# Optimization experiments

Measured on AMD Instinct MI355X. Metric: run time of the kernel, lower is better.

## Reference

```python
import jax, jax.numpy as jnp
import numpy as np

N, C, H, W = 32, 512, 32, 32
D = C // 2  # theta/phi embed channels


def setup_inputs() -> dict:
    key = jax.random.key(0)
    ks = jax.random.split(key, 7)
    s = 0.05
    return {
        "x": jax.random.normal(ks[0], (N, C, H, W), jnp.float32),
        "W_theta": jax.random.normal(ks[1], (D, C), jnp.float32) * s,
        "b_theta": jax.random.normal(ks[2], (D,), jnp.float32) * s,
        "W_phi": jax.random.normal(ks[3], (D, C), jnp.float32) * s,
        "b_phi": jax.random.normal(ks[4], (D,), jnp.float32) * s,
        "W_fuse": jax.random.normal(ks[5], (C, C), jnp.float32) * s,
        "b_fuse": jax.random.normal(ks[6], (C,), jnp.float32) * s,
    }


def _conv1x1(x, Wt, bt):
    # 1x1 conv == per-pixel linear: [n,c,h,w] x [o,c] -> [n,o,h,w]
    return jnp.einsum('nchw,oc->nohw', x, Wt) + bt[None, :, None, None]


def reference(x, W_theta, b_theta, W_phi, b_phi, W_fuse, b_fuse):
    n, c, h, w = x.shape
    theta = _conv1x1(x, W_theta, b_theta)          # [n, d, h, w]
    phi = _conv1x1(x, W_phi, b_phi)                # [n, d, h, w]
    d = theta.shape[1]
    hw = h * w
    t = theta.reshape(n, d, hw)                    # queries [n, d, hw]
    p = phi.reshape(n, d, hw)                      # keys    [n, d, hw]
    g = x.reshape(n, c, hw)                        # values  [n, c, hw]
    scale = 1.0 / np.sqrt(float(d))
    f = jnp.einsum('ndq,ndk->nqk', t, p) * scale   # [n, hw, hw]
    f = jax.nn.softmax(f, axis=-1)
    attn = jnp.einsum('nqk,nck->ncq', f, g).reshape(n, c, h, w)
    return x + _conv1x1(attn, W_fuse, b_fuse)
```

## Files before the change

kernel.cpp:

```cpp
#include <hip/hip_runtime.h>


#define NB  32
#define CC  512
#define HWD 1024

typedef __attribute__((ext_vector_type(8))) short short8;
typedef __attribute__((ext_vector_type(4))) float f32x4;

__device__ __forceinline__ unsigned short f2bu(float f) {
    unsigned int u = __float_as_uint(f);
    u = (u + 0x7FFFu + ((u >> 16) & 1u)) >> 16;
    return (unsigned short)u;
}

__global__ __launch_bounds__(256) void k_packw(const float* __restrict__ Wt,
                                               const float* __restrict__ Wp,
                                               const float* __restrict__ Wf,
                                               unsigned short* __restrict__ Wcat,
                                               unsigned short* __restrict__ Wfuse) {
    int idx = blockIdx.x * 256 + threadIdx.x;
    int o = idx >> 9;
    float cv = (o < 256) ? Wt[idx] : Wp[idx - 131072];
    Wcat[idx]  = f2bu(cv);
    Wfuse[idx] = f2bu(Wf[idx]);
}

__global__ __launch_bounds__(512) void k_mm(const float* __restrict__ x,
                                            const unsigned short* __restrict__ Wcat,
                                            const unsigned short* __restrict__ Wfuse,
                                            const float* __restrict__ bt,
                                            const float* __restrict__ bp,
                                            unsigned short* __restrict__ tp,
                                            unsigned short* __restrict__ Z) {
    __shared__ __align__(16) float Tr[32 * 132];
    __shared__ __align__(16) unsigned short As[128 * 40];
    __shared__ __align__(16) unsigned short Bs[256 * 40];
    const int m0 = blockIdx.x << 7;
    const int yb = blockIdx.y;
    const bool isZ = (yb >= 2);
    const int n0 = (yb & 1) << 8;
    const unsigned short* W = isZ ? Wfuse : Wcat;
    const int n  = m0 >> 10, qbase = m0 & 1023;
    const int t = threadIdx.x, lane = t & 63, wave = t >> 6;
    const int wr = wave >> 2, wc = wave & 3;
    const int lrow = lane & 15, hi = lane >> 4, lhk = hi << 3;
    const f32x4 fz = {0.f, 0.f, 0.f, 0.f};
    f32x4 acc[4][4];
#pragma unroll
    for (int i = 0; i < 4; ++i)
#pragma unroll
        for (int j = 0; j < 4; ++j) acc[i][j] = fz;

    const int tr_r = t >> 4, tr_q = (t & 15) << 3;
    const int p2_pix = t & 127, p2_c = (t >> 7) << 3;

    for (int kt = 0; kt < 16; ++kt) {
        const int k0 = kt << 5;
        {
            const float* src = x + ((size_t)(n * CC + k0 + tr_r)) * HWD + qbase + tr_q;
            float4 v0 = *(const float4*)(src);
            float4 v1 = *(const float4*)(src + 4);
            *(float4*)(Tr + tr_r * 132 + tr_q) = v0;
            *(float4*)(Tr + tr_r * 132 + tr_q + 4) = v1;
#pragma unroll
            for (int i = 0; i < 2; ++i) {
                int chunk = t + (i << 9);
                int r = chunk >> 2, ko = (chunk & 3) << 3;
                *(uint4*)(Bs + r * 40 + ko) =
                    *(const uint4*)(W + ((size_t)(n0 + r)) * CC + k0 + ko);
            }
        }
        __syncthreads();
        {
            short8 o8;
#pragma unroll
            for (int j = 0; j < 8; ++j)
                o8[j] = (short)f2bu(Tr[(p2_c + j) * 132 + p2_pix]);
            *(short8*)(As + p2_pix * 40 + p2_c) = o8;
        }
        __syncthreads();
        short8 af[4], bfm[4];
#pragma unroll
        for (int mi = 0; mi < 4; ++mi)
            af[mi] = *(const short8*)(As + (wr * 64 + mi * 16 + lrow) * 40 + lhk);
#pragma unroll
        for (int ni = 0; ni < 4; ++ni)
            bfm[ni] = *(const short8*)(Bs + (wc * 64 + ni * 16 + lrow) * 40 + lhk);
#pragma unroll
        for (int mi = 0; mi < 4; ++mi)
#pragma unroll
            for (int ni = 0; ni < 4; ++ni)
                acc[mi][ni] = __builtin_amdgcn_mfma_f32_16x16x32_bf16(
                    af[mi], bfm[ni], acc[mi][ni], 0, 0, 0);
        __syncthreads();
    }
    if (!isZ) {
#pragma unroll
        for (int ni = 0; ni < 4; ++ni) {
            const int col = n0 + wc * 64 + ni * 16 + lrow;
            const float bias = (col < 256) ? bt[col] : bp[col - 256];
#pragma unroll
            for (int mi = 0; mi < 4; ++mi)
#pragma unroll
                for (int j = 0; j < 4; ++j) {
                    const int row = m0 + wr * 64 + mi * 16 + hi * 4 + j;
                    tp[(size_t)row * CC + col] = f2bu(acc[mi][ni][j] + bias);
                }
        }
    } else {
        const int kbase = qbase + wr * 64;
        unsigned short* Zn = Z + (size_t)n * CC * HWD;
#pragma unroll
        for (int ni = 0; ni < 4; ++ni) {
            const int o = n0 + wc * 64 + ni * 16 + lrow;
#pragma unroll
            for (int mi = 0; mi < 4; ++mi) {
                ushort4 v;
                v.x = f2bu(acc[mi][ni][0]);
                v.y = f2bu(acc[mi][ni][1]);
                v.z = f2bu(acc[mi][ni][2]);
                v.w = f2bu(acc[mi][ni][3]);
                *(ushort4*)(Zn + (size_t)o * HWD + kbase + mi * 16 + (hi << 2)) = v;
            }
        }
    }
}

__global__ __launch_bounds__(512, 2) void k_attn8(const unsigned short* __restrict__ tp,
                                                  const unsigned short* __restrict__ Z,
                                                  const float* __restrict__ bfu,
                                                  const float* __restrict__ x,
                                                  float* __restrict__ out) {
    constexpr int QST = 264;
    constexpr int PST = 264;
    constexpr int QSZ = 128 * QST;
    __shared__ __align__(16) unsigned short SL[QSZ + 128 * PST];
    __shared__ float rowsum[128];
    unsigned short* Qs = SL;
    unsigned short* P  = SL + QSZ;

    const int b = blockIdx.x;
    const int n = b & 31;
    const int q0 = (b >> 5) << 7;
    const int t = threadIdx.x, lane = t & 63, wave = t >> 6;
    const int lrow = lane & 15, hi = lane >> 4, lhk = hi << 3;
    const f32x4 fz = {0.f, 0.f, 0.f, 0.f};

    const unsigned short* tpn = tp + (size_t)n * HWD * CC;
    const unsigned short* Zn  = Z + (size_t)n * CC * HWD;

    if (t < 128) rowsum[t] = 0.f;
#pragma unroll
    for (int pass = 0; pass < 8; ++pass) {
        int chunk = (pass << 9) + t;
        int row = chunk >> 5, co = (chunk & 31) << 3;
        *(short8*)(Qs + row * QST + co) =
            *(const short8*)(tpn + (size_t)(q0 + row) * CC + co);
    }
    __syncthreads();

    f32x4 accG[8][4];
#pragma unroll
    for (int qj = 0; qj < 8; ++qj)
#pragma unroll
        for (int mi = 0; mi < 4; ++mi) accG[qj][mi] = fz;

    const int kw = wave << 4;
    const int ob = wave << 6;

    for (int it = 0; it < 4; ++it) {
        const int kv0 = it << 8;
        const size_t krow0 = (size_t)(kv0 + kw + lrow) * CC + 256;
        const size_t krow1 = (size_t)(kv0 + 128 + kw + lrow) * CC + 256;
        f32x4 accA[2][8];
#pragma unroll
        for (int k2 = 0; k2 < 2; ++k2)
#pragma unroll
            for (int qj = 0; qj < 8; ++qj) accA[k2][qj] = fz;
#pragma unroll
        for (int kt = 0; kt < 8; ++kt) {
            const int d0 = (kt << 5) + lhk;
            short8 kf0 = *(const short8*)(tpn + krow0 + d0);
            short8 kf1 = *(const short8*)(tpn + krow1 + d0);
#pragma unroll
            for (int qj = 0; qj < 8; ++qj) {
                short8 qfr = *(const short8*)(Qs + (qj * 16 + lrow) * QST + d0);
                accA[0][qj] = __builtin_amdgcn_mfma_f32_16x16x32_bf16(qfr, kf0, accA[0][qj], 0, 0, 0);
                accA[1][qj] = __builtin_amdgcn_mfma_f32_16x16x32_bf16(qfr, kf1, accA[1][qj], 0, 0, 0);
            }
        }
        float psum[8][4];
#pragma unroll
        for (int qj = 0; qj < 8; ++qj)
#pragma unroll
            for (int j = 0; j < 4; ++j) psum[qj][j] = 0.f;
#pragma unroll
        for (int k2 = 0; k2 < 2; ++k2) {
            const int pcol = (k2 << 7) + kw + lrow;
#pragma unroll
            for (int qj = 0; qj < 8; ++qj)
#pragma unroll
                for (int j = 0; j < 4; ++j) {
                    float p = __expf(accA[k2][qj][j] * 0.0625f);
                    psum[qj][j] += p;
                    P[(qj * 16 + hi * 4 + j) * PST + pcol] = f2bu(p);
                }
        }
#pragma unroll
        for (int qj = 0; qj < 8; ++qj)
#pragma unroll
            for (int j = 0; j < 4; ++j) {
                float s = psum[qj][j];
                s += __shfl_xor(s, 1, 16);
                s += __shfl_xor(s, 2, 16);
                s += __shfl_xor(s, 4, 16);
                s += __shfl_xor(s, 8, 16);
                if (lrow == 0) atomicAdd(&rowsum[qj * 16 + hi * 4 + j], s);
            }
        __syncthreads();
        __builtin_amdgcn_s_setprio(1);
#pragma unroll
        for (int ks = 0; ks < 8; ++ks) {
            const int kb = (ks << 5) + lhk;
            short8 zf[4];
#pragma unroll
            for (int mi = 0; mi < 4; ++mi)
                zf[mi] = *(const short8*)(Zn + (size_t)(ob + mi * 16 + lrow) * HWD + kv0 + kb);
#pragma unroll
            for (int qj = 0; qj < 8; ++qj) {
                short8 pa = *(const short8*)(P + (qj * 16 + lrow) * PST + kb);
#pragma unroll
                for (int mi = 0; mi < 4; ++mi)
                    accG[qj][mi] = __builtin_amdgcn_mfma_f32_16x16x32_bf16(
                        pa, zf[mi], accG[qj][mi], 0, 0, 0);
            }
        }
        __builtin_amdgcn_s_setprio(0);
        __syncthreads();
    }

    if (t < 128) rowsum[t] = 1.f / rowsum[t];
    __syncthreads();
    float bias[4];
#pragma unroll
    for (int mi = 0; mi < 4; ++mi) bias[mi] = bfu[ob + mi * 16 + lrow];
#pragma unroll
    for (int qj = 0; qj < 8; ++qj) {
        const float4 inv4 = *(const float4*)&rowsum[qj * 16 + (hi << 2)];
#pragma unroll
        for (int mi = 0; mi < 4; ++mi) {
            const int o = ob + mi * 16 + lrow;
            const size_t idx = ((size_t)(n * CC + o)) * HWD + q0 + qj * 16 + (hi << 2);
            const float4 xr = *(const float4*)(x + idx);
            float4 r;
            r.x = accG[qj][mi][0] * inv4.x + bias[mi] + xr.x;
            r.y = accG[qj][mi][1] * inv4.y + bias[mi] + xr.y;
            r.z = accG[qj][mi][2] * inv4.z + bias[mi] + xr.z;
            r.w = accG[qj][mi][3] * inv4.w + bias[mi] + xr.w;
            *(float4*)(out + idx) = r;
        }
    }
}

extern "C" void kernel_launch(void* const* d_in, const int* in_sizes, int n_in,
                              void* d_out, int out_size, void* d_ws, size_t ws_size,
                              hipStream_t stream) {
    const float* x  = (const float*)d_in[0];
    const float* Wt = (const float*)d_in[1];
    const float* bt = (const float*)d_in[2];
    const float* Wp = (const float*)d_in[3];
    const float* bp = (const float*)d_in[4];
    const float* Wf = (const float*)d_in[5];
    const float* bfu = (const float*)d_in[6];
    float* out = (float*)d_out;

    char* ws = (char*)d_ws;
    unsigned short* tp    = (unsigned short*)(ws);
    unsigned short* Z     = (unsigned short*)(ws + 33554432);
    unsigned short* Wcat  = (unsigned short*)(ws + 67108864);
    unsigned short* Wfuse = (unsigned short*)(ws + 67633152);

    k_packw<<<dim3(1024), 256, 0, stream>>>(Wt, Wp, Wf, Wcat, Wfuse);
    k_mm   <<<dim3(256, 4), 512, 0, stream>>>(x, Wcat, Wfuse, bt, bp, tp, Z);
    k_attn8<<<dim3(256), 512, 0, stream>>>(tp, Z, bfu, x, out);
}
```

Measured before the change: 170.4 us.

## Prefetch next K and Z fragments across barriers, defer rowsum reduction

The attention kernel now prefetches the first two K-fragment slices for the next kv tile and the first Z fragment before and around the barrier, so global loads overlap the barrier wait and the start of MFMA work. Row-sum partials are kept in registers across all kv tiles and reduced with shuffles and LDS atomics once at the end rather than every iteration. Barriers are replaced with a lighter macro that waits only on LDS counters plus a scheduling fence. This adds register pressure under a 512x2 launch bound, which could cause spills or lower occupancy.

```diff
diff --git a/kernel.cpp b/kernel.cpp
--- a/kernel.cpp
+++ b/kernel.cpp
@@ -7,6 +7,12 @@
 
 typedef __attribute__((ext_vector_type(8))) short short8;
 typedef __attribute__((ext_vector_type(4))) float f32x4;
+
+#define LBAR() do {                                            \
+    asm volatile("s_waitcnt lgkmcnt(0)" ::: "memory");         \
+    __builtin_amdgcn_s_barrier();                              \
+    __builtin_amdgcn_sched_barrier(0);                         \
+} while (0)
 
 __device__ __forceinline__ unsigned short f2bu(float f) {
     unsigned int u = __float_as_uint(f);
@@ -127,7 +133,7 @@
     }
 }
 
-__global__ __launch_bounds__(512, 2) void k_attn8(const unsigned short* __restrict__ tp,
+__global__ __launch_bounds__(512, 2) void k_attn9(const unsigned short* __restrict__ tp,
                                                   const unsigned short* __restrict__ Z,
                                                   const float* __restrict__ bfu,
                                                   const float* __restrict__ x,
@@ -158,16 +164,31 @@
         *(short8*)(Qs + row * QST + co) =
             *(const short8*)(tpn + (size_t)(q0 + row) * CC + co);
     }
-    __syncthreads();
+    LBAR();
 
     f32x4 accG[8][4];
 #pragma unroll
     for (int qj = 0; qj < 8; ++qj)
 #pragma unroll
         for (int mi = 0; mi < 4; ++mi) accG[qj][mi] = fz;
+    float psum[8][4];
+#pragma unroll
+    for (int qj = 0; qj < 8; ++qj)
+#pragma unroll
+        for (int j = 0; j < 4; ++j) psum[qj][j] = 0.f;
 
     const int kw = wave << 4;
     const int ob = wave << 6;
+
+    short8 kpre[2][2];
+    {
+        const size_t kr0 = (size_t)(kw + lrow) * CC + 256;
+        const size_t kr1 = (size_t)(128 + kw + lrow) * CC + 256;
+        kpre[0][0] = *(const short8*)(tpn + kr0 + lhk);
+        kpre[0][1] = *(const short8*)(tpn + kr1 + lhk);
+        kpre[1][0] = *(const short8*)(tpn + kr0 + 32 + lhk);
+        kpre[1][1] = *(const short8*)(tpn + kr1 + 32 + lhk);
+    }
 
     for (int it = 0; it < 4; ++it) {
         const int kv0 = it << 8;
@@ -181,8 +202,12 @@
 #pragma unroll
         for (int kt = 0; kt < 8; ++kt) {
             const int d0 = (kt << 5) + lhk;
-            short8 kf0 = *(const short8*)(tpn + krow0 + d0);
-            short8 kf1 = *(const short8*)(tpn + krow1 + d0);
+            short8 kf0, kf1;
+            if (kt < 2) { kf0 = kpre[kt][0]; kf1 = kpre[kt][1]; }
+            else {
+                kf0 = *(const short8*)(tpn + krow0 + d0);
+                kf1 = *(const short8*)(tpn + krow1 + d0);
+            }
 #pragma unroll
             for (int qj = 0; qj < 8; ++qj) {
                 short8 qfr = *(const short8*)(Qs + (qj * 16 + lrow) * QST + d0);
@@ -190,11 +215,6 @@
                 accA[1][qj] = __builtin_amdgcn_mfma_f32_16x16x32_bf16(qfr, kf1, accA[1][qj], 0, 0, 0);
             }
         }
-        float psum[8][4];
-#pragma unroll
-        for (int qj = 0; qj < 8; ++qj)
-#pragma unroll
-            for (int j = 0; j < 4; ++j) psum[qj][j] = 0.f;
 #pragma unroll
         for (int k2 = 0; k2 < 2; ++k2) {
             const int pcol = (k2 << 7) + kw + lrow;
@@ -207,26 +227,32 @@
                     P[(qj * 16 + hi * 4 + j) * PST + pcol] = f2bu(p);
                 }
         }
-#pragma unroll
-        for (int qj = 0; qj < 8; ++qj)
-#pragma unroll
-            for (int j = 0; j < 4; ++j) {
-                float s = psum[qj][j];
-                s += __shfl_xor(s, 1, 16);
-                s += __shfl_xor(s, 2, 16);
-                s += __shfl_xor(s, 4, 16);
-                s += __shfl_xor(s, 8, 16);
-                if (lrow == 0) atomicAdd(&rowsum[qj * 16 + hi * 4 + j], s);
-            }
-        __syncthreads();
+        short8 zpre[4];
+#pragma unroll
+        for (int mi = 0; mi < 4; ++mi)
+            zpre[mi] = *(const short8*)(Zn + (size_t)(ob + mi * 16 + lrow) * HWD + kv0 + lhk);
+        LBAR();
+        if (it < 3) {
+            const size_t nr0 = (size_t)(kv0 + 256 + kw + lrow) * CC + 256;
+            const size_t nr1 = (size_t)(kv0 + 384 + kw + lrow) * CC + 256;
+            kpre[0][0] = *(const short8*)(tpn + nr0 + lhk);
+            kpre[0][1] = *(const short8*)(tpn + nr1 + lhk);
+            kpre[1][0] = *(const short8*)(tpn + nr0 + 32 + lhk);
+            kpre[1][1] = *(const short8*)(tpn + nr1 + 32 + lhk);
+        }
         __builtin_amdgcn_s_setprio(1);
 #pragma unroll
         for (int ks = 0; ks < 8; ++ks) {
             const int kb = (ks << 5) + lhk;
             short8 zf[4];
-#pragma unroll
-            for (int mi = 0; mi < 4; ++mi)
-                zf[mi] = *(const short8*)(Zn + (size_t)(ob + mi * 16 + lrow) * HWD + kv0 + kb);
+            if (ks == 0) {
+#pragma unroll
+                for (int mi = 0; mi < 4; ++mi) zf[mi] = zpre[mi];
+            } else {
+#pragma unroll
+                for (int mi = 0; mi < 4; ++mi)
+                    zf[mi] = *(const short8*)(Zn + (size_t)(ob + mi * 16 + lrow) * HWD + kv0 + kb);
+            }
 #pragma unroll
             for (int qj = 0; qj < 8; ++qj) {
                 short8 pa = *(const short8*)(P + (qj * 16 + lrow) * PST + kb);
@@ -237,11 +263,24 @@
             }
         }
         __builtin_amdgcn_s_setprio(0);
-        __syncthreads();
-    }
+        LBAR();
+    }
+
+#pragma unroll
+    for (int qj = 0; qj < 8; ++qj)
+#pragma unroll
+        for (int j = 0; j < 4; ++j) {
+            float s = psum[qj][j];
+            s += __shfl_xor(s, 1, 16);
+            s += __shfl_xor(s, 2, 16);
+            s += __shfl_xor(s, 4, 16);
+            s += __shfl_xor(s, 8, 16);
+            if (lrow == 0) atomicAdd(&rowsum[qj * 16 + hi * 4 + j], s);
+        }
+    LBAR();
 
     if (t < 128) rowsum[t] = 1.f / rowsum[t];
-    __syncthreads();
+    LBAR();
     float bias[4];
 #pragma unroll
     for (int mi = 0; mi < 4; ++mi) bias[mi] = bfu[ob + mi * 16 + lrow];
@@ -283,5 +322,5 @@
 
     k_packw<<<dim3(1024), 256, 0, stream>>>(Wt, Wp, Wf, Wcat, Wfuse);
     k_mm   <<<dim3(256, 4), 512, 0, stream>>>(x, Wcat, Wfuse, bt, bp, tp, Z);
-    k_attn8<<<dim3(256), 512, 0, stream>>>(tp, Z, bfu, x, out);
-}
+    k_attn9<<<dim3(256), 512, 0, stream>>>(tp, Z, bfu, x, out);
+}
```

New measurement: 190.4 us. +11.7%, slower.

## Compute theta/phi and fused Z projections in one block sharing the x tile

Applied to the files above, without the earlier changes.

Each block of the projection GEMM now computes both the theta/phi embedding and the W_fuse-projected values for the same pixel/channel tile, reusing the transposed bf16 x tile for two sets of MFMAs. This halves the reads and conversions of x and the grid size (1024 to 512 blocks), and remaps block indices to group tiles. The cost is double the accumulator registers and extra shared memory for a second weight tile, with launch bounds forcing one block per CU, which may lower occupancy.

```diff
diff --git a/kernel.cpp b/kernel.cpp
--- a/kernel.cpp
+++ b/kernel.cpp
@@ -26,31 +26,32 @@
     Wfuse[idx] = f2bu(Wf[idx]);
 }
 
-__global__ __launch_bounds__(512) void k_mm(const float* __restrict__ x,
-                                            const unsigned short* __restrict__ Wcat,
-                                            const unsigned short* __restrict__ Wfuse,
-                                            const float* __restrict__ bt,
-                                            const float* __restrict__ bp,
-                                            unsigned short* __restrict__ tp,
-                                            unsigned short* __restrict__ Z) {
+__global__ __launch_bounds__(512, 1) void k_mm2(const float* __restrict__ x,
+                                                const unsigned short* __restrict__ Wcat,
+                                                const unsigned short* __restrict__ Wfuse,
+                                                const float* __restrict__ bt,
+                                                const float* __restrict__ bp,
+                                                unsigned short* __restrict__ tp,
+                                                unsigned short* __restrict__ Z) {
     __shared__ __align__(16) float Tr[32 * 132];
     __shared__ __align__(16) unsigned short As[128 * 40];
     __shared__ __align__(16) unsigned short Bs[256 * 40];
-    const int m0 = blockIdx.x << 7;
-    const int yb = blockIdx.y;
-    const bool isZ = (yb >= 2);
-    const int n0 = (yb & 1) << 8;
-    const unsigned short* W = isZ ? Wfuse : Wcat;
+    __shared__ __align__(16) unsigned short Bs2[256 * 40];
+    const int b = blockIdx.x;
+    const int bx = ((b >> 4) << 3) | (b & 7);
+    const int yb = (b >> 3) & 1;
+    const int m0 = bx << 7;
+    const int n0 = yb << 8;
     const int n  = m0 >> 10, qbase = m0 & 1023;
     const int t = threadIdx.x, lane = t & 63, wave = t >> 6;
     const int wr = wave >> 2, wc = wave & 3;
     const int lrow = lane & 15, hi = lane >> 4, lhk = hi << 3;
     const f32x4 fz = {0.f, 0.f, 0.f, 0.f};
-    f32x4 acc[4][4];
+    f32x4 accE[4][4], accZ[4][4];
 #pragma unroll
     for (int i = 0; i < 4; ++i)
 #pragma unroll
-        for (int j = 0; j < 4; ++j) acc[i][j] = fz;
+        for (int j = 0; j < 4; ++j) { accE[i][j] = fz; accZ[i][j] = fz; }
 
     const int tr_r = t >> 4, tr_q = (t & 15) << 3;
     const int p2_pix = t & 127, p2_c = (t >> 7) << 3;
@@ -68,7 +69,9 @@
                 int chunk = t + (i << 9);
                 int r = chunk >> 2, ko = (chunk & 3) << 3;
                 *(uint4*)(Bs + r * 40 + ko) =
-                    *(const uint4*)(W + ((size_t)(n0 + r)) * CC + k0 + ko);
+                    *(const uint4*)(Wcat + ((size_t)(n0 + r)) * CC + k0 + ko);
+                *(uint4*)(Bs2 + r * 40 + ko) =
+                    *(const uint4*)(Wfuse + ((size_t)(n0 + r)) * CC + k0 + ko);
             }
         }
         __syncthreads();
@@ -91,38 +94,44 @@
         for (int mi = 0; mi < 4; ++mi)
 #pragma unroll
             for (int ni = 0; ni < 4; ++ni)
-                acc[mi][ni] = __builtin_amdgcn_mfma_f32_16x16x32_bf16(
-                    af[mi], bfm[ni], acc[mi][ni], 0, 0, 0);
-        __syncthreads();
-    }
-    if (!isZ) {
-#pragma unroll
-        for (int ni = 0; ni < 4; ++ni) {
-            const int col = n0 + wc * 64 + ni * 16 + lrow;
-            const float bias = (col < 256) ? bt[col] : bp[col - 256];
-#pragma unroll
-            for (int mi = 0; mi < 4; ++mi)
-#pragma unroll
-                for (int j = 0; j < 4; ++j) {
-                    const int row = m0 + wr * 64 + mi * 16 + hi * 4 + j;
-                    tp[(size_t)row * CC + col] = f2bu(acc[mi][ni][j] + bias);
-                }
-        }
-    } else {
-        const int kbase = qbase + wr * 64;
-        unsigned short* Zn = Z + (size_t)n * CC * HWD;
-#pragma unroll
-        for (int ni = 0; ni < 4; ++ni) {
-            const int o = n0 + wc * 64 + ni * 16 + lrow;
-#pragma unroll
-            for (int mi = 0; mi < 4; ++mi) {
-                ushort4 v;
-                v.x = f2bu(acc[mi][ni][0]);
-                v.y = f2bu(acc[mi][ni][1]);
-                v.z = f2bu(acc[mi][ni][2]);
-                v.w = f2bu(acc[mi][ni][3]);
-                *(ushort4*)(Zn + (size_t)o * HWD + kbase + mi * 16 + (hi << 2)) = v;
-            }
+                accE[mi][ni] = __builtin_amdgcn_mfma_f32_16x16x32_bf16(
+                    af[mi], bfm[ni], accE[mi][ni], 0, 0, 0);
+#pragma unroll
+        for (int ni = 0; ni < 4; ++ni)
+            bfm[ni] = *(const short8*)(Bs2 + (wc * 64 + ni * 16 + lrow) * 40 + lhk);
+#pragma unroll
+        for (int mi = 0; mi < 4; ++mi)
+#pragma unroll
+            for (int ni = 0; ni < 4; ++ni)
+                accZ[mi][ni] = __builtin_amdgcn_mfma_f32_16x16x32_bf16(
+                    af[mi], bfm[ni], accZ[mi][ni], 0, 0, 0);
+        __syncthreads();
+    }
+#pragma unroll
+    for (int ni = 0; ni < 4; ++ni) {
+        const int col = n0 + wc * 64 + ni * 16 + lrow;
+        const float bias = (col < 256) ? bt[col] : bp[col - 256];
+#pragma unroll
+        for (int mi = 0; mi < 4; ++mi)
+#pragma unroll
+            for (int j = 0; j < 4; ++j) {
+                const int row = m0 + wr * 64 + mi * 16 + hi * 4 + j;
+                tp[(size_t)row * CC + col] = f2bu(accE[mi][ni][j] + bias);
+            }
+    }
+    const int kbase = qbase + wr * 64;
+    unsigned short* Zn = Z + (size_t)n * CC * HWD;
+#pragma unroll
+    for (int ni = 0; ni < 4; ++ni) {
+        const int o = n0 + wc * 64 + ni * 16 + lrow;
+#pragma unroll
+        for (int mi = 0; mi < 4; ++mi) {
+            ushort4 v;
+            v.x = f2bu(accZ[mi][ni][0]);
+            v.y = f2bu(accZ[mi][ni][1]);
+            v.z = f2bu(accZ[mi][ni][2]);
+            v.w = f2bu(accZ[mi][ni][3]);
+            *(ushort4*)(Zn + (size_t)o * HWD + kbase + mi * 16 + (hi << 2)) = v;
         }
     }
 }
@@ -282,6 +291,6 @@
     unsigned short* Wfuse = (unsigned short*)(ws + 67633152);
 
     k_packw<<<dim3(1024), 256, 0, stream>>>(Wt, Wp, Wf, Wcat, Wfuse);
-    k_mm   <<<dim3(256, 4), 512, 0, stream>>>(x, Wcat, Wfuse, bt, bp, tp, Z);
+    k_mm2  <<<dim3(512), 512, 0, stream>>>(x, Wcat, Wfuse, bt, bp, tp, Z);
     k_attn8<<<dim3(256), 512, 0, stream>>>(tp, Z, bfu, x, out);
 }
```

Result: slower. 182.5 us (+7.0%).

## Split fused attention into separate score-softmax and PV GEMM kernels

Applied to the files above, without the earlier changes.

Replaces the fused attention kernel with two tiled GEMM kernels. k_S computes exponentiated scores, writes them as bf16 to global memory and accumulates row sums with global atomics. k_ZP then multiplies Z by P and applies the normalisation, bias and residual. The batch is processed in two halves so the score buffers can reuse free space in the output buffer and in already-consumed workspace. This gives more blocks and simpler GEMM tiles, but adds a large round trip of the score matrix through global memory plus more launches.

```diff
diff --git a/kernel.cpp b/kernel.cpp
--- a/kernel.cpp
+++ b/kernel.cpp
@@ -18,12 +18,14 @@
                                                const float* __restrict__ Wp,
                                                const float* __restrict__ Wf,
                                                unsigned short* __restrict__ Wcat,
-                                               unsigned short* __restrict__ Wfuse) {
+                                               unsigned short* __restrict__ Wfuse,
+                                               float* __restrict__ rowsumG) {
     int idx = blockIdx.x * 256 + threadIdx.x;
     int o = idx >> 9;
     float cv = (o < 256) ? Wt[idx] : Wp[idx - 131072];
     Wcat[idx]  = f2bu(cv);
     Wfuse[idx] = f2bu(Wf[idx]);
+    if (idx < 32768) rowsumG[idx] = 0.f;
 }
 
 __global__ __launch_bounds__(512) void k_mm(const float* __restrict__ x,
@@ -127,139 +129,154 @@
     }
 }
 
-__global__ __launch_bounds__(512, 2) void k_attn8(const unsigned short* __restrict__ tp,
-                                                  const unsigned short* __restrict__ Z,
-                                                  const float* __restrict__ bfu,
-                                                  const float* __restrict__ x,
-                                                  float* __restrict__ out) {
-    constexpr int QST = 264;
-    constexpr int PST = 264;
-    constexpr int QSZ = 128 * QST;
-    __shared__ __align__(16) unsigned short SL[QSZ + 128 * PST];
-    __shared__ float rowsum[128];
-    unsigned short* Qs = SL;
-    unsigned short* P  = SL + QSZ;
-
-    const int b = blockIdx.x;
-    const int n = b & 31;
-    const int q0 = (b >> 5) << 7;
+__global__ __launch_bounds__(256) void k_S(const unsigned short* __restrict__ tpH,
+                                           unsigned short* __restrict__ Pb0,
+                                           unsigned short* __restrict__ Pb1,
+                                           float* __restrict__ rsH) {
+    __shared__ __align__(16) unsigned short As[128 * 40];
+    __shared__ __align__(16) unsigned short Bs[128 * 40];
+    __shared__ float rs[128];
+    const int m0 = blockIdx.x << 7;
+    const int k0b = blockIdx.y << 7;
+    const int nl = blockIdx.z;
+    const unsigned short* tpn = tpH + (size_t)nl * HWD * CC;
+    unsigned short* Pn = (nl < 8) ? (Pb0 + (size_t)nl * HWD * HWD)
+                                  : (Pb1 + (size_t)(nl - 8) * HWD * HWD);
     const int t = threadIdx.x, lane = t & 63, wave = t >> 6;
+    const int wr = wave >> 1, wc = wave & 1;
     const int lrow = lane & 15, hi = lane >> 4, lhk = hi << 3;
     const f32x4 fz = {0.f, 0.f, 0.f, 0.f};
-
-    const unsigned short* tpn = tp + (size_t)n * HWD * CC;
-    const unsigned short* Zn  = Z + (size_t)n * CC * HWD;
-
-    if (t < 128) rowsum[t] = 0.f;
-#pragma unroll
-    for (int pass = 0; pass < 8; ++pass) {
-        int chunk = (pass << 9) + t;
-        int row = chunk >> 5, co = (chunk & 31) << 3;
-        *(short8*)(Qs + row * QST + co) =
-            *(const short8*)(tpn + (size_t)(q0 + row) * CC + co);
-    }
+    f32x4 acc[4][4];
+#pragma unroll
+    for (int i = 0; i < 4; ++i)
+#pragma unroll
+        for (int j = 0; j < 4; ++j) acc[i][j] = fz;
+    if (t < 128) rs[t] = 0.f;
+
+    for (int kt = 0; kt < 8; ++kt) {
+        const int k0 = kt << 5;
+#pragma unroll
+        for (int i = 0; i < 2; ++i) {
+            int chunk = t + (i << 8);
+            int r = chunk >> 2, ko = (chunk & 3) << 3;
+            *(uint4*)(As + r * 40 + ko) =
+                *(const uint4*)(tpn + (size_t)(m0 + r) * CC + k0 + ko);
+            *(uint4*)(Bs + r * 40 + ko) =
+                *(const uint4*)(tpn + (size_t)(k0b + r) * CC + 256 + k0 + ko);
+        }
+        __syncthreads();
+        short8 af[4], bfm[4];
+#pragma unroll
+        for (int mi = 0; mi < 4; ++mi)
+            af[mi] = *(const short8*)(As + (wr * 64 + mi * 16 + lrow) * 40 + lhk);
+#pragma unroll
+        for (int ni = 0; ni < 4; ++ni)
+            bfm[ni] = *(const short8*)(Bs + (wc * 64 + ni * 16 + lrow) * 40 + lhk);
+#pragma unroll
+        for (int mi = 0; mi < 4; ++mi)
+#pragma unroll
+            for (int ni = 0; ni < 4; ++ni)
+                acc[mi][ni] = __builtin_amdgcn_mfma_f32_16x16x32_bf16(
+                    af[mi], bfm[ni], acc[mi][ni], 0, 0, 0);
+        __syncthreads();
+    }
+    float sloc[4][4];
+#pragma unroll
+    for (int mi = 0; mi < 4; ++mi)
+#pragma unroll
+        for (int j = 0; j < 4; ++j) sloc[mi][j] = 0.f;
+#pragma unroll
+    for (int ni = 0; ni < 4; ++ni) {
+        const int kc = k0b + wc * 64 + ni * 16 + lrow;
+#pragma unroll
+        for (int mi = 0; mi < 4; ++mi)
+#pragma unroll
+            for (int j = 0; j < 4; ++j) {
+                const int row = m0 + wr * 64 + mi * 16 + hi * 4 + j;
+                float p = __expf(acc[mi][ni][j] * 0.0625f);
+                sloc[mi][j] += p;
+                Pn[(size_t)row * HWD + kc] = f2bu(p);
+            }
+    }
+#pragma unroll
+    for (int mi = 0; mi < 4; ++mi)
+#pragma unroll
+        for (int j = 0; j < 4; ++j) {
+            float s = sloc[mi][j];
+            s += __shfl_xor(s, 1, 16);
+            s += __shfl_xor(s, 2, 16);
+            s += __shfl_xor(s, 4, 16);
+            s += __shfl_xor(s, 8, 16);
+            if (lrow == 0) atomicAdd(&rs[wr * 64 + mi * 16 + hi * 4 + j], s);
+        }
     __syncthreads();
-
-    f32x4 accG[8][4];
-#pragma unroll
-    for (int qj = 0; qj < 8; ++qj)
-#pragma unroll
-        for (int mi = 0; mi < 4; ++mi) accG[qj][mi] = fz;
-
-    const int kw = wave << 4;
-    const int ob = wave << 6;
-
-    for (int it = 0; it < 4; ++it) {
-        const int kv0 = it << 8;
-        const size_t krow0 = (size_t)(kv0 + kw + lrow) * CC + 256;
-        const size_t krow1 = (size_t)(kv0 + 128 + kw + lrow) * CC + 256;
-        f32x4 accA[2][8];
-#pragma unroll
-        for (int k2 = 0; k2 < 2; ++k2)
-#pragma unroll
-            for (int qj = 0; qj < 8; ++qj) accA[k2][qj] = fz;
-#pragma unroll
-        for (int kt = 0; kt < 8; ++kt) {
-            const int d0 = (kt << 5) + lhk;
-            short8 kf0 = *(const short8*)(tpn + krow0 + d0);
-            short8 kf1 = *(const short8*)(tpn + krow1 + d0);
-#pragma unroll
-            for (int qj = 0; qj < 8; ++qj) {
-                short8 qfr = *(const short8*)(Qs + (qj * 16 + lrow) * QST + d0);
-                accA[0][qj] = __builtin_amdgcn_mfma_f32_16x16x32_bf16(qfr, kf0, accA[0][qj], 0, 0, 0);
-                accA[1][qj] = __builtin_amdgcn_mfma_f32_16x16x32_bf16(qfr, kf1, accA[1][qj], 0, 0, 0);
+    if (t < 128) atomicAdd(&rsH[(size_t)nl * HWD + m0 + t], rs[t]);
+}
+
+__global__ __launch_bounds__(256) void k_ZP(const unsigned short* __restrict__ ZH,
+                                            const unsigned short* __restrict__ Pb0,
+                                            const unsigned short* __restrict__ Pb1,
+                                            const float* __restrict__ rsH,
+                                            const float* __restrict__ bfu,
+                                            const float* __restrict__ xH,
+                                            float* __restrict__ outH) {
+    __shared__ __align__(16) unsigned short As[128 * 40];
+    __shared__ __align__(16) unsigned short Bs[128 * 40];
+    const int q0 = blockIdx.x << 7;
+    const int o0 = blockIdx.y << 7;
+    const int nl = blockIdx.z;
+    const unsigned short* Zn = ZH + (size_t)nl * CC * HWD;
+    const unsigned short* Pn = (nl < 8) ? (Pb0 + (size_t)nl * HWD * HWD)
+                                        : (Pb1 + (size_t)(nl - 8) * HWD * HWD);
+    const int t = threadIdx.x, lane = t & 63, wave = t >> 6;
+    const int wr = wave >> 1, wc = wave & 1;
+    const int lrow = lane & 15, hi = lane >> 4, lhk = hi << 3;
+    const f32x4 fz = {0.f, 0.f, 0.f, 0.f};
+    f32x4 acc[4][4];
+#pragma unroll
+    for (int i = 0; i < 4; ++i)
+#pragma unroll
+        for (int j = 0; j < 4; ++j) acc[i][j] = fz;
+
+    for (int kt = 0; kt < 32; ++kt) {
+        const int k0 = kt << 5;
+#pragma unroll
+        for (int i = 0; i < 2; ++i) {
+            int chunk = t + (i << 8);
+            int r = chunk >> 2, ko = (chunk & 3) << 3;
+            *(uint4*)(As + r * 40 + ko) =
+                *(const uint4*)(Zn + (size_t)(o0 + r) * HWD + k0 + ko);
+            *(uint4*)(Bs + r * 40 + ko) =
+                *(const uint4*)(Pn + (size_t)(q0 + r) * HWD + k0 + ko);
+        }
+        __syncthreads();
+        short8 af[4], bfm[4];
+#pragma unroll
+        for (int mi = 0; mi < 4; ++mi)
+            af[mi] = *(const short8*)(As + (wr * 64 + mi * 16 + lrow) * 40 + lhk);
+#pragma unroll
+        for (int ni = 0; ni < 4; ++ni)
+            bfm[ni] = *(const short8*)(Bs + (wc * 64 + ni * 16 + lrow) * 40 + lhk);
+#pragma unroll
+        for (int mi = 0; mi < 4; ++mi)
+#pragma unroll
+            for (int ni = 0; ni < 4; ++ni)
+                acc[mi][ni] = __builtin_amdgcn_mfma_f32_16x16x32_bf16(
+                    af[mi], bfm[ni], acc[mi][ni], 0, 0, 0);
+        __syncthreads();
+    }
+#pragma unroll
+    for (int ni = 0; ni < 4; ++ni) {
+        const int qc = q0 + wc * 64 + ni * 16 + lrow;
+        const float inv = 1.f / rsH[(size_t)nl * HWD + qc];
+#pragma unroll
+        for (int mi = 0; mi < 4; ++mi)
+#pragma unroll
+            for (int j = 0; j < 4; ++j) {
+                const int o = o0 + wr * 64 + mi * 16 + hi * 4 + j;
+                const size_t idx = ((size_t)(nl * CC + o)) * HWD + qc;
+                outH[idx] = acc[mi][ni][j] * inv + bfu[o] + xH[idx];
             }
-        }
-        float psum[8][4];
-#pragma unroll
-        for (int qj = 0; qj < 8; ++qj)
-#pragma unroll
-            for (int j = 0; j < 4; ++j) psum[qj][j] = 0.f;
-#pragma unroll
-        for (int k2 = 0; k2 < 2; ++k2) {
-            const int pcol = (k2 << 7) + kw + lrow;
-#pragma unroll
-            for (int qj = 0; qj < 8; ++qj)
-#pragma unroll
-                for (int j = 0; j < 4; ++j) {
-                    float p = __expf(accA[k2][qj][j] * 0.0625f);
-                    psum[qj][j] += p;
-                    P[(qj * 16 + hi * 4 + j) * PST + pcol] = f2bu(p);
-                }
-        }
-#pragma unroll
-        for (int qj = 0; qj < 8; ++qj)
-#pragma unroll
-            for (int j = 0; j < 4; ++j) {
-                float s = psum[qj][j];
-                s += __shfl_xor(s, 1, 16);
-                s += __shfl_xor(s, 2, 16);
-                s += __shfl_xor(s, 4, 16);
-                s += __shfl_xor(s, 8, 16);
-                if (lrow == 0) atomicAdd(&rowsum[qj * 16 + hi * 4 + j], s);
-            }
-        __syncthreads();
-        __builtin_amdgcn_s_setprio(1);
-#pragma unroll
-        for (int ks = 0; ks < 8; ++ks) {
-            const int kb = (ks << 5) + lhk;
-            short8 zf[4];
-#pragma unroll
-            for (int mi = 0; mi < 4; ++mi)
-                zf[mi] = *(const short8*)(Zn + (size_t)(ob + mi * 16 + lrow) * HWD + kv0 + kb);
-#pragma unroll
-            for (int qj = 0; qj < 8; ++qj) {
-                short8 pa = *(const short8*)(P + (qj * 16 + lrow) * PST + kb);
-#pragma unroll
-                for (int mi = 0; mi < 4; ++mi)
-                    accG[qj][mi] = __builtin_amdgcn_mfma_f32_16x16x32_bf16(
-                        pa, zf[mi], accG[qj][mi], 0, 0, 0);
-            }
-        }
-        __builtin_amdgcn_s_setprio(0);
-        __syncthreads();
-    }
-
-    if (t < 128) rowsum[t] = 1.f / rowsum[t];
-    __syncthreads();
-    float bias[4];
-#pragma unroll
-    for (int mi = 0; mi < 4; ++mi) bias[mi] = bfu[ob + mi * 16 + lrow];
-#pragma unroll
-    for (int qj = 0; qj < 8; ++qj) {
-        const float4 inv4 = *(const float4*)&rowsum[qj * 16 + (hi << 2)];
-#pragma unroll
-        for (int mi = 0; mi < 4; ++mi) {
-            const int o = ob + mi * 16 + lrow;
-            const size_t idx = ((size_t)(n * CC + o)) * HWD + q0 + qj * 16 + (hi << 2);
-            const float4 xr = *(const float4*)(x + idx);
-            float4 r;
-            r.x = accG[qj][mi][0] * inv4.x + bias[mi] + xr.x;
-            r.y = accG[qj][mi][1] * inv4.y + bias[mi] + xr.y;
-            r.z = accG[qj][mi][2] * inv4.z + bias[mi] + xr.z;
-            r.w = accG[qj][mi][3] * inv4.w + bias[mi] + xr.w;
-            *(float4*)(out + idx) = r;
-        }
     }
 }
 
@@ -280,8 +297,25 @@
     unsigned short* Z     = (unsigned short*)(ws + 33554432);
     unsigned short* Wcat  = (unsigned short*)(ws + 67108864);
     unsigned short* Wfuse = (unsigned short*)(ws + 67633152);
-
-    k_packw<<<dim3(1024), 256, 0, stream>>>(Wt, Wp, Wf, Wcat, Wfuse);
+    float*          rsG   = (float*)(ws + 68157440);
+
+    const size_t HB = (size_t)16 * HWD * CC;
+
+    k_packw<<<dim3(1024), 256, 0, stream>>>(Wt, Wp, Wf, Wcat, Wfuse, rsG);
     k_mm   <<<dim3(256, 4), 512, 0, stream>>>(x, Wcat, Wfuse, bt, bp, tp, Z);
-    k_attn8<<<dim3(256), 512, 0, stream>>>(tp, Z, bfu, x, out);
-}
+
+    {
+        unsigned short* P0 = (unsigned short*)(out + (size_t)8 * 1024 * 1024);
+        unsigned short* P0b = P0 + (size_t)8 * HWD * HWD;
+        k_S <<<dim3(8, 8, 16), 256, 0, stream>>>(tp, P0, P0b, rsG);
+        k_ZP<<<dim3(8, 4, 16), 256, 0, stream>>>(Z, P0, P0b, rsG, bfu, x, out);
+    }
+    {
+        unsigned short* P1a = (unsigned short*)(ws);
+        unsigned short* P1b = (unsigned short*)(ws + 33554432);
+        k_S <<<dim3(8, 8, 16), 256, 0, stream>>>(tp + HB, P1a, P1b, rsG + 16 * HWD);
+        k_ZP<<<dim3(8, 4, 16), 256, 0, stream>>>(Z + HB, P1a, P1b, rsG + 16 * HWD,
+                                                 bfu, x + (size_t)16 * CC * HWD,
+                                                 out + (size_t)16 * CC * HWD);
+    }
+}
```

Measured after the change: 231.3 us. 1.36x slower.
